# Optimization experiments

Measured on AMD Instinct MI355X. Metric: run time of the kernel, lower is better.

The kernel has to match this reference:

```python
import jax, jax.numpy as jnp
import numpy as np

N_HEADS = 16
ROPE_THETA = 10000.0


def setup_inputs() -> dict:
    key = jax.random.key(0)
    k1, k2, k3 = jax.random.split(key, 3)
    B, T, C = 1, 4096, 1024
    d_k = C // N_HEADS
    x = jax.random.normal(k1, (B, T, C), dtype=jnp.float32)
    # RoPE frequencies: freqs_cis = exp(i * t * theta^{-2j/d_k}), stored as cos/sin
    inv_freq = 1.0 / (ROPE_THETA ** (jnp.arange(0, d_k, 2, dtype=jnp.float32) / d_k))  # (d_k//2,)
    t = jnp.arange(T, dtype=jnp.float32)
    angles = jnp.outer(t, inv_freq)  # (T, d_k//2)
    freqs_cos = jnp.cos(angles)
    freqs_sin = jnp.sin(angles)
    W_attn = jax.random.normal(k2, (C, 3 * C), dtype=jnp.float32) * 0.02  # x @ W_attn == Linear(C,3C,bias=False)
    W_proj = jax.random.normal(k3, (C, C), dtype=jnp.float32) * 0.02
    return {"x": x, "freqs_cos": freqs_cos, "freqs_sin": freqs_sin, "W_attn": W_attn, "W_proj": W_proj}


def _rope(x, cos, sin):
    # x: (B, H, T, d_k); cos/sin: (T, d_k//2). Interleaved-pair rotation
    # matching torch.view_as_complex on (..., d_k//2, 2).
    xr = x.reshape(*x.shape[:-1], -1, 2)
    x0, x1 = xr[..., 0], xr[..., 1]
    c = cos[None, None, :, :]
    s = sin[None, None, :, :]
    o0 = x0 * c - x1 * s
    o1 = x0 * s + x1 * c
    return jnp.stack([o0, o1], axis=-1).reshape(x.shape)


def reference(x, freqs_cos, freqs_sin, W_attn, W_proj):
    B, T, C = x.shape
    H = N_HEADS
    d_k = C // H
    qkv = x @ W_attn  # (B, T, 3C)
    q, k, v = jnp.split(qkv, 3, axis=-1)
    q = q.reshape(B, T, H, d_k).transpose(0, 2, 1, 3)  # (B, H, T, d_k)
    k = k.reshape(B, T, H, d_k).transpose(0, 2, 1, 3)
    v = v.reshape(B, T, H, d_k).transpose(0, 2, 1, 3)
    q = _rope(q, freqs_cos[:T], freqs_sin[:T])
    k = _rope(k, freqs_cos[:T], freqs_sin[:T])
    scale = 1.0 / jnp.sqrt(jnp.asarray(d_k, dtype=x.dtype))
    att = jnp.einsum("bhqd,bhkd->bhqk", q, k) * scale  # (B, H, T, T)
    causal = jnp.tril(jnp.ones((T, T), dtype=bool))
    att = jnp.where(causal[None, None, :, :], att, -jnp.inf)
    att = jax.nn.softmax(att, axis=-1)
    y = jnp.einsum("bhqk,bhkd->bhqd", att, v)  # (B, H, T, d_k)
    y = y.transpose(0, 2, 1, 3).reshape(B, T, C)
    return y @ W_proj
```

## Files before the change

kernel.cpp:

```cpp
#include <hip/hip_runtime.h>

using f32x4  = __attribute__((ext_vector_type(4))) float;
using bf16x4 = __attribute__((ext_vector_type(4))) __bf16;
using bf16x8 = __attribute__((ext_vector_type(8))) __bf16;
using s16x4  = __attribute__((ext_vector_type(4))) short;

__device__ inline void gload16(const void* g, void* l) {
  __builtin_amdgcn_global_load_lds((const __attribute__((address_space(1))) void*)g,
                                   (__attribute__((address_space(3))) void*)l, 16, 0, 0);
}

__device__ inline f32x4 mfma16x16x16bf(bf16x4 a, bf16x4 b, f32x4 c) {
#if __has_builtin(__builtin_amdgcn_mfma_f32_16x16x16_bf16)
  return __builtin_amdgcn_mfma_f32_16x16x16_bf16(a, b, c, 0, 0, 0);
#else
  return __builtin_amdgcn_mfma_f32_16x16x16bf16_1k(__builtin_bit_cast(s16x4, a),
                                                   __builtin_bit_cast(s16x4, b), c, 0, 0, 0);
#endif
}

__global__ __launch_bounds__(256) void pack_bf16_kernel(const float* __restrict__ in,
                                                        __bf16* __restrict__ out, int n4) {
  int i = blockIdx.x * 256 + threadIdx.x;
  if (i >= n4) return;
  f32x4 v = ((const f32x4*)in)[i];
  bf16x4 o;
  o[0] = (__bf16)v[0]; o[1] = (__bf16)v[1]; o[2] = (__bf16)v[2]; o[3] = (__bf16)v[3];
  ((bf16x4*)out)[i] = o;
}

__global__ __launch_bounds__(256) void transpose_bf16_kernel(const float* __restrict__ in,
                                                             __bf16* __restrict__ out,
                                                             int R, int C) {
  __shared__ float tile[32][33];
  int c0 = blockIdx.x * 32, r0 = blockIdx.y * 32;
  int tx = threadIdx.x, ty = threadIdx.y;
  #pragma unroll
  for (int i = 0; i < 32; i += 8)
    tile[ty + i][tx] = in[(size_t)(r0 + ty + i) * C + c0 + tx];
  __syncthreads();
  #pragma unroll
  for (int i = 0; i < 32; i += 8)
    out[(size_t)(c0 + ty + i) * R + r0 + tx] = (__bf16)tile[tx][ty + i];
}

template <typename OUT>
__global__ __launch_bounds__(256) void gemm_bt_kernel(const __bf16* __restrict__ A,
                                                      const __bf16* __restrict__ Bt,
                                                      OUT* __restrict__ C,
                                                      int M, int N, int K) {
  const int nwg = gridDim.x, flat = blockIdx.x;
  const int cpx = nwg >> 3;
  const int wg = (flat & 7) * cpx + (flat >> 3);
  const int nbn = N >> 7;
  const int bn = (wg % nbn) * 128, bm = (wg / nbn) * 128;

  const int tid = threadIdx.x;
  const int lane = tid & 63, wid = tid >> 6;
  const int wm = (wid >> 1) * 64, wn = (wid & 1) * 64;
  const int l15 = lane & 15, lhi = lane >> 4;
  __shared__ __align__(16) __bf16 As[2][4096];
  __shared__ __align__(16) __bf16 Bs[2][4096];
  f32x4 acc[4][4] = {};

  const int rrow = wid * 16 + (lane >> 2);
  const int schunk = lane & 3;

  #define G_STAGE(k0_, b_)                                                              \
    {                                                                                   \
      _Pragma("unroll")                                                                 \
      for (int i_ = 0; i_ < 2; ++i_) {                                                  \
        int row_ = i_ * 64 + rrow;                                                      \
        int lch_ = schunk ^ (row_ & 3);                                                 \
        gload16(A + (size_t)(bm + row_) * K + (k0_) + lch_ * 8,                         \
                (char*)&As[b_][0] + i_ * 4096 + wid * 1024);                            \
        gload16(Bt + (size_t)(bn + row_) * K + (k0_) + lch_ * 8,                        \
                (char*)&Bs[b_][0] + i_ * 4096 + wid * 1024);                            \
      }                                                                                 \
    }

  G_STAGE(0, 0);
  __syncthreads();
  const int nk = K >> 5;
  for (int t = 0; t < nk; ++t) {
    const int cur = t & 1;
    if (t + 1 < nk) G_STAGE((t + 1) * 32, cur ^ 1);
    bf16x8 af[4], bfr[4];
    #pragma unroll
    for (int i = 0; i < 4; ++i) {
      int row = wm + i * 16 + l15;
      af[i] = *(const bf16x8*)&As[cur][row * 32 + ((lhi ^ (row & 3)) * 8)];
    }
    #pragma unroll
    for (int j = 0; j < 4; ++j) {
      int row = wn + j * 16 + l15;
      bfr[j] = *(const bf16x8*)&Bs[cur][row * 32 + ((lhi ^ (row & 3)) * 8)];
    }
    #pragma unroll
    for (int i = 0; i < 4; ++i)
      #pragma unroll
      for (int j = 0; j < 4; ++j)
        acc[i][j] = __builtin_amdgcn_mfma_f32_16x16x32_bf16(af[i], bfr[j], acc[i][j], 0, 0, 0);
    __syncthreads();
  }
  #pragma unroll
  for (int i = 0; i < 4; ++i)
    #pragma unroll
    for (int j = 0; j < 4; ++j)
      #pragma unroll
      for (int r = 0; r < 4; ++r)
        C[(size_t)(bm + wm + i * 16 + lhi * 4 + r) * N + (bn + wn + j * 16 + l15)] =
            (OUT)acc[i][j][r];
  #undef G_STAGE
}

__global__ __launch_bounds__(256) void postproc_kernel(const __bf16* __restrict__ qkv,
                                                       const float* __restrict__ fc,
                                                       const float* __restrict__ fs,
                                                       __bf16* __restrict__ qb,
                                                       __bf16* __restrict__ kst,
                                                       __bf16* __restrict__ vst) {
  const int ktile = blockIdx.x, h = blockIdx.y;
  const int tid = threadIdx.x;
  const int row = tid >> 2, seg = tid & 3;
  const int t = ktile * 64 + row;
  __shared__ __bf16 vt[64][72];

  float cs[8], sn[8];
  #pragma unroll
  for (int p = 0; p < 8; ++p) {
    cs[p] = fc[t * 32 + seg * 8 + p];
    sn[p] = fs[t * 32 + seg * 8 + p];
  }
  const float QS = 0.125f * 1.4426950408889634f;

  {
    const __bf16* src = qkv + (size_t)t * 3072 + h * 64 + seg * 16;
    bf16x8 a = *(const bf16x8*)src, b = *(const bf16x8*)(src + 8);
    float v[16];
    #pragma unroll
    for (int i = 0; i < 8; ++i) { v[i] = (float)a[i]; v[8 + i] = (float)b[i]; }
    __bf16 ob[16];
    #pragma unroll
    for (int p = 0; p < 8; ++p) {
      ob[2 * p]     = (__bf16)((v[2 * p] * cs[p] - v[2 * p + 1] * sn[p]) * QS);
      ob[2 * p + 1] = (__bf16)((v[2 * p] * sn[p] + v[2 * p + 1] * cs[p]) * QS);
    }
    __bf16* dst = qb + (size_t)t * 1024 + h * 64 + seg * 16;
    *(bf16x8*)dst = *(bf16x8*)ob;
    *(bf16x8*)(dst + 8) = *(bf16x8*)(ob + 8);
  }
  {
    const __bf16* src = qkv + (size_t)t * 3072 + 1024 + h * 64 + seg * 16;
    bf16x8 a = *(const bf16x8*)src, b = *(const bf16x8*)(src + 8);
    float v[16];
    #pragma unroll
    for (int i = 0; i < 8; ++i) { v[i] = (float)a[i]; v[8 + i] = (float)b[i]; }
    __bf16 ob[16];
    #pragma unroll
    for (int p = 0; p < 8; ++p) {
      ob[2 * p]     = (__bf16)(v[2 * p] * cs[p] - v[2 * p + 1] * sn[p]);
      ob[2 * p + 1] = (__bf16)(v[2 * p] * sn[p] + v[2 * p + 1] * cs[p]);
    }
    __bf16* kdst = kst + ((size_t)(h * 64 + ktile)) * 4096 + row * 64;
    const int r7 = row & 7;
    *(bf16x8*)(kdst + ((seg * 2) ^ r7) * 8)     = *(bf16x8*)ob;
    *(bf16x8*)(kdst + ((seg * 2 + 1) ^ r7) * 8) = *(bf16x8*)(ob + 8);
  }
  {
    const __bf16* src = qkv + (size_t)t * 3072 + 2048 + h * 64 + seg * 16;
    *(bf16x8*)&vt[row][seg * 16]     = *(const bf16x8*)src;
    *(bf16x8*)&vt[row][seg * 16 + 8] = *(const bf16x8*)(src + 8);
  }
  __syncthreads();
  {
    const int d = tid >> 2, q4 = tid & 3;
    __bf16 tb[16];
    #pragma unroll
    for (int j = 0; j < 16; ++j) tb[j] = vt[q4 * 16 + j][d];
    __bf16* vdst = vst + ((size_t)(h * 64 + ktile)) * 4096 + d * 64;
    const int r7 = d & 7;
    *(bf16x8*)(vdst + ((q4 * 2) ^ r7) * 8)     = *(bf16x8*)tb;
    *(bf16x8*)(vdst + ((q4 * 2 + 1) ^ r7) * 8) = *(bf16x8*)(tb + 8);
  }
}

__global__ __launch_bounds__(256) void fattn_kernel(const __bf16* __restrict__ qb,
                                                    const __bf16* __restrict__ kst,
                                                    const __bf16* __restrict__ vst,
                                                    __bf16* __restrict__ yb) {
  const int b = blockIdx.x;
  const int xcd = b & 7, slot = b >> 3;
  const int head = xcd * 2 + (slot & 1);
  const int qt = 63 - (slot >> 1);
  const int tid = threadIdx.x, lane = tid & 63, w = tid >> 6;
  const int c16 = lane & 15, g = lane >> 4;

  __shared__ __align__(16) __bf16 kls[2][4096];
  __shared__ __align__(16) __bf16 vls[2][4096];

  const __bf16* ktiles = kst + (size_t)head * 64 * 4096;
  const __bf16* vtiles = vst + (size_t)head * 64 * 4096;

  #define F_STAGE(kt_, b_)                                                        \
    {                                                                             \
      const char* kb_ = (const char*)(ktiles + (size_t)(kt_) * 4096);             \
      const char* vb_ = (const char*)(vtiles + (size_t)(kt_) * 4096);             \
      _Pragma("unroll")                                                           \
      for (int i_ = 0; i_ < 2; ++i_) {                                            \
        int off_ = i_ * 4096 + w * 1024;                                          \
        gload16(kb_ + off_ + lane * 16, (char*)&kls[b_][0] + off_);               \
        gload16(vb_ + off_ + lane * 16, (char*)&vls[b_][0] + off_);               \
      }                                                                           \
    }

  const int qw0 = qt * 64 + w * 16;

  bf16x8 qf[2];
  #pragma unroll
  for (int kc = 0; kc < 2; ++kc)
    qf[kc] = *(const bf16x8*)(qb + (size_t)(qw0 + c16) * 1024 + head * 64 + kc * 32 + g * 8);

  f32x4 o[4] = {};
  f32x4 ol = {};
  bf16x4 ones1;
  ones1[0] = ones1[1] = ones1[2] = ones1[3] = (__bf16)1.0f;

  const int m7 = c16 & 7, h2 = g >> 1, lo4 = (g & 1) * 4;
  const __bf16* kp0 = &kls[0][c16 * 64 + ((g ^ m7) * 8)];
  const __bf16* kp1 = &kls[0][c16 * 64 + (((4 + g) ^ m7) * 8)];
  const __bf16* vp0 = &vls[0][c16 * 64 + lo4 + (((0 + h2) ^ m7) * 8)];
  const __bf16* vp1 = &vls[0][c16 * 64 + lo4 + (((2 + h2) ^ m7) * 8)];
  const __bf16* vp2 = &vls[0][c16 * 64 + lo4 + (((4 + h2) ^ m7) * 8)];
  const __bf16* vp3 = &vls[0][c16 * 64 + lo4 + (((6 + h2) ^ m7) * 8)];

  #define F_ONE_ST(B_, st_, vp_)                                                  \
    {                                                                             \
      bf16x4 pv;                                                                  \
      _Pragma("unroll")                                                           \
      for (int r = 0; r < 4; ++r) pv[r] = (__bf16)exp2f(s[st_][r]);               \
      __builtin_amdgcn_s_setprio(1);                                              \
      ol = mfma16x16x16bf(ones1, pv, ol);                                         \
      _Pragma("unroll")                                                           \
      for (int dt = 0; dt < 4; ++dt) {                                            \
        bf16x4 va = *(const bf16x4*)(vp_ + (B_) * 4096 + dt * 1024);              \
        o[dt] = mfma16x16x16bf(va, pv, o[dt]);                                    \
      }                                                                           \
      __builtin_amdgcn_s_setprio(0);                                              \
    }

  #define F_COMPUTE(B_, kt_)                                                      \
    {                                                                             \
      f32x4 s[4];                                                                 \
      __builtin_amdgcn_s_setprio(1);                                              \
      _Pragma("unroll")                                                           \
      for (int st = 0; st < 4; ++st) {                                            \
        bf16x8 ka0 = *(const bf16x8*)(kp0 + (B_) * 4096 + st * 1024);             \
        bf16x8 ka1 = *(const bf16x8*)(kp1 + (B_) * 4096 + st * 1024);             \
        f32x4 z = {};                                                             \
        z = __builtin_amdgcn_mfma_f32_16x16x32_bf16(ka0, qf[0], z, 0, 0, 0);      \
        s[st] = __builtin_amdgcn_mfma_f32_16x16x32_bf16(ka1, qf[1], z, 0, 0, 0);  \
      }                                                                           \
      __builtin_amdgcn_s_setprio(0);                                              \
      if ((kt_) == qt) {                                                          \
        const int qloc = w * 16 + c16;                                            \
        _Pragma("unroll")                                                         \
        for (int st = 0; st < 4; ++st)                                            \
          _Pragma("unroll")                                                       \
          for (int r = 0; r < 4; ++r)                                             \
            if (st * 16 + g * 4 + r > qloc) s[st][r] = -1e30f;                    \
      }                                                                           \
      F_ONE_ST(B_, 0, vp0)                                                        \
      F_ONE_ST(B_, 1, vp1)                                                        \
      F_ONE_ST(B_, 2, vp2)                                                        \
      F_ONE_ST(B_, 3, vp3)                                                        \
    }

  F_STAGE(0, 0);
  __syncthreads();

  int kt = 0;
  while (true) {
    if (kt < qt) F_STAGE(kt + 1, 1);
    F_COMPUTE(0, kt)
    __syncthreads();
    if (kt == qt) break;
    ++kt;
    if (kt < qt) F_STAGE(kt + 1, 0);
    F_COMPUTE(1, kt)
    __syncthreads();
    if (kt == qt) break;
    ++kt;
  }

  const float inv = 1.f / ol[0];
  const int q = qw0 + c16;
  #pragma unroll
  for (int dt = 0; dt < 4; ++dt) {
    bf16x4 ov;
    #pragma unroll
    for (int r = 0; r < 4; ++r) ov[r] = (__bf16)(o[dt][r] * inv);
    *(bf16x4*)(yb + (size_t)q * 1024 + head * 64 + dt * 16 + g * 4) = ov;
  }
  #undef F_STAGE
  #undef F_COMPUTE
  #undef F_ONE_ST
}

extern "C" void kernel_launch(void* const* d_in, const int* in_sizes, int n_in,
                              void* d_out, int out_size, void* d_ws, size_t ws_size,
                              hipStream_t stream) {
  const float* x  = (const float*)d_in[0];
  const float* fc = (const float*)d_in[1];
  const float* fs = (const float*)d_in[2];
  const float* Wa = (const float*)d_in[3];
  const float* Wp = (const float*)d_in[4];
  float* out = (float*)d_out;

  char* ws = (char*)d_ws;
  __bf16* x_bf   = (__bf16*)(ws);
  __bf16* Wa_t   = (__bf16*)(ws + 8388608);
  __bf16* Wp_t   = (__bf16*)(ws + 14680064);
  __bf16* y_bf   = (__bf16*)(ws + 16777216);
  __bf16* qkv_bf = (__bf16*)(ws + 25165824);
  __bf16* kst    = (__bf16*)(ws + 50331648);
  __bf16* vst    = (__bf16*)(ws + 58720256);
  __bf16* q_bf   = x_bf;

  pack_bf16_kernel<<<4096, 256, 0, stream>>>(x, x_bf, 1048576);
  transpose_bf16_kernel<<<dim3(96, 32), dim3(32, 8), 0, stream>>>(Wa, Wa_t, 1024, 3072);
  transpose_bf16_kernel<<<dim3(32, 32), dim3(32, 8), 0, stream>>>(Wp, Wp_t, 1024, 1024);
  gemm_bt_kernel<__bf16><<<768, 256, 0, stream>>>(x_bf, Wa_t, qkv_bf, 4096, 3072, 1024);
  postproc_kernel<<<dim3(64, 16), 256, 0, stream>>>(qkv_bf, fc, fs, q_bf, kst, vst);
  fattn_kernel<<<1024, 256, 0, stream>>>(q_bf, kst, vst, y_bf);
  gemm_bt_kernel<float><<<256, 256, 0, stream>>>(y_bf, Wp_t, out, 4096, 1024, 1024);
}
```

Baseline: 225.1 us.

## Split long causal attention rows across two blocks and fuse prep kernels

Query tiles 31..63 are now each split into two key-range halves handled by separate blocks. Those blocks write unnormalized fp32 partial outputs and row sums, which a new combine kernel adds and normalizes into the bf16 output. This is meant to even out the causal load imbalance, where late query tiles dominate the tail. It also merges the pack and two transpose kernels into one launch to cut launch overhead. In exchange it adds an extra kernel, partial-result traffic, and reuses the qkv buffer region for the partials.

```diff
diff --git a/kernel.cpp b/kernel.cpp
--- a/kernel.cpp
+++ b/kernel.cpp
@@ -19,22 +19,31 @@
 #endif
 }
 
-__global__ __launch_bounds__(256) void pack_bf16_kernel(const float* __restrict__ in,
-                                                        __bf16* __restrict__ out, int n4) {
-  int i = blockIdx.x * 256 + threadIdx.x;
-  if (i >= n4) return;
-  f32x4 v = ((const f32x4*)in)[i];
-  bf16x4 o;
-  o[0] = (__bf16)v[0]; o[1] = (__bf16)v[1]; o[2] = (__bf16)v[2]; o[3] = (__bf16)v[3];
-  ((bf16x4*)out)[i] = o;
-}
-
-__global__ __launch_bounds__(256) void transpose_bf16_kernel(const float* __restrict__ in,
-                                                             __bf16* __restrict__ out,
-                                                             int R, int C) {
+__global__ __launch_bounds__(256) void prep_kernel(const float* __restrict__ x,
+                                                   const float* __restrict__ Wa,
+                                                   const float* __restrict__ Wp,
+                                                   __bf16* __restrict__ x_bf,
+                                                   __bf16* __restrict__ Wa_t,
+                                                   __bf16* __restrict__ Wp_t) {
+  const int b = blockIdx.x, tid = threadIdx.x;
+  if (b < 4096) {
+    int i = b * 256 + tid;
+    f32x4 v = ((const f32x4*)x)[i];
+    bf16x4 o;
+    o[0] = (__bf16)v[0]; o[1] = (__bf16)v[1]; o[2] = (__bf16)v[2]; o[3] = (__bf16)v[3];
+    ((bf16x4*)x_bf)[i] = o;
+    return;
+  }
   __shared__ float tile[32][33];
-  int c0 = blockIdx.x * 32, r0 = blockIdx.y * 32;
-  int tx = threadIdx.x, ty = threadIdx.y;
+  const int tx = tid & 31, ty = tid >> 5;
+  const float* in; __bf16* out; int R, C, c0, r0;
+  if (b < 4096 + 3072) {
+    int bx = b - 4096; in = Wa; out = Wa_t; R = 1024; C = 3072;
+    c0 = (bx % 96) * 32; r0 = (bx / 96) * 32;
+  } else {
+    int bx = b - 7168; in = Wp; out = Wp_t; R = 1024; C = 1024;
+    c0 = (bx & 31) * 32; r0 = (bx >> 5) * 32;
+  }
   #pragma unroll
   for (int i = 0; i < 32; i += 8)
     tile[ty + i][tx] = in[(size_t)(r0 + ty + i) * C + c0 + tx];
@@ -188,11 +197,26 @@
 __global__ __launch_bounds__(256) void fattn_kernel(const __bf16* __restrict__ qb,
                                                     const __bf16* __restrict__ kst,
                                                     const __bf16* __restrict__ vst,
-                                                    __bf16* __restrict__ yb) {
+                                                    __bf16* __restrict__ yb,
+                                                    float* __restrict__ opart,
+                                                    float* __restrict__ lpart) {
   const int b = blockIdx.x;
-  const int xcd = b & 7, slot = b >> 3;
-  const int head = xcd * 2 + (slot & 1);
-  const int qt = 63 - (slot >> 1);
+  const int xcd = b & 7, s = b >> 3;
+  const int head = xcd * 2 + (s & 1);
+  const int slot = s >> 1;
+  int qt, kt0, kt1, part, pid = 0;
+  if (slot < 66) {
+    qt = 63 - (slot >> 1);
+    part = slot & 1;
+    const int h1 = (qt + 1) >> 1;
+    kt0 = part ? h1 : 0;
+    kt1 = part ? qt : h1 - 1;
+    pid = (head * 33 + (qt - 31)) * 2 + part;
+  } else {
+    qt = 30 - (slot - 66);
+    part = -1;
+    kt0 = 0; kt1 = qt;
+  }
   const int tid = threadIdx.x, lane = tid & 63, w = tid >> 6;
   const int c16 = lane & 15, g = lane >> 4;
 
@@ -238,7 +262,7 @@
     {                                                                             \
       bf16x4 pv;                                                                  \
       _Pragma("unroll")                                                           \
-      for (int r = 0; r < 4; ++r) pv[r] = (__bf16)exp2f(s[st_][r]);               \
+      for (int r = 0; r < 4; ++r) pv[r] = (__bf16)exp2f(s_[st_][r]);              \
       __builtin_amdgcn_s_setprio(1);                                              \
       ol = mfma16x16x16bf(ones1, pv, ol);                                         \
       _Pragma("unroll")                                                           \
@@ -251,7 +275,7 @@
 
   #define F_COMPUTE(B_, kt_)                                                      \
     {                                                                             \
-      f32x4 s[4];                                                                 \
+      f32x4 s_[4];                                                                \
       __builtin_amdgcn_s_setprio(1);                                              \
       _Pragma("unroll")                                                           \
       for (int st = 0; st < 4; ++st) {                                            \
@@ -259,7 +283,7 @@
         bf16x8 ka1 = *(const bf16x8*)(kp1 + (B_) * 4096 + st * 1024);             \
         f32x4 z = {};                                                             \
         z = __builtin_amdgcn_mfma_f32_16x16x32_bf16(ka0, qf[0], z, 0, 0, 0);      \
-        s[st] = __builtin_amdgcn_mfma_f32_16x16x32_bf16(ka1, qf[1], z, 0, 0, 0);  \
+        s_[st] = __builtin_amdgcn_mfma_f32_16x16x32_bf16(ka1, qf[1], z, 0, 0, 0); \
       }                                                                           \
       __builtin_amdgcn_s_setprio(0);                                              \
       if ((kt_) == qt) {                                                          \
@@ -268,7 +292,7 @@
         for (int st = 0; st < 4; ++st)                                            \
           _Pragma("unroll")                                                       \
           for (int r = 0; r < 4; ++r)                                             \
-            if (st * 16 + g * 4 + r > qloc) s[st][r] = -1e30f;                    \
+            if (st * 16 + g * 4 + r > qloc) s_[st][r] = -1e30f;                   \
       }                                                                           \
       F_ONE_ST(B_, 0, vp0)                                                        \
       F_ONE_ST(B_, 1, vp1)                                                        \
@@ -276,35 +300,65 @@
       F_ONE_ST(B_, 3, vp3)                                                        \
     }
 
-  F_STAGE(0, 0);
+  F_STAGE(kt0, 0);
   __syncthreads();
 
-  int kt = 0;
+  int kt = kt0;
   while (true) {
-    if (kt < qt) F_STAGE(kt + 1, 1);
+    if (kt < kt1) F_STAGE(kt + 1, 1);
     F_COMPUTE(0, kt)
     __syncthreads();
-    if (kt == qt) break;
+    if (kt == kt1) break;
     ++kt;
-    if (kt < qt) F_STAGE(kt + 1, 0);
+    if (kt < kt1) F_STAGE(kt + 1, 0);
     F_COMPUTE(1, kt)
     __syncthreads();
-    if (kt == qt) break;
+    if (kt == kt1) break;
     ++kt;
   }
 
-  const float inv = 1.f / ol[0];
-  const int q = qw0 + c16;
-  #pragma unroll
-  for (int dt = 0; dt < 4; ++dt) {
-    bf16x4 ov;
-    #pragma unroll
-    for (int r = 0; r < 4; ++r) ov[r] = (__bf16)(o[dt][r] * inv);
-    *(bf16x4*)(yb + (size_t)q * 1024 + head * 64 + dt * 16 + g * 4) = ov;
+  if (part >= 0) {
+    float* Op = opart + (size_t)pid * 4096 + (w * 16 + c16) * 64;
+    #pragma unroll
+    for (int dt = 0; dt < 4; ++dt)
+      *(f32x4*)(Op + dt * 16 + g * 4) = o[dt];
+    if (g == 0) lpart[pid * 64 + w * 16 + c16] = ol[0];
+  } else {
+    const float inv = 1.f / ol[0];
+    const int q = qw0 + c16;
+    #pragma unroll
+    for (int dt = 0; dt < 4; ++dt) {
+      bf16x4 ov;
+      #pragma unroll
+      for (int r = 0; r < 4; ++r) ov[r] = (__bf16)(o[dt][r] * inv);
+      *(bf16x4*)(yb + (size_t)q * 1024 + head * 64 + dt * 16 + g * 4) = ov;
+    }
   }
   #undef F_STAGE
   #undef F_COMPUTE
   #undef F_ONE_ST
+}
+
+__global__ __launch_bounds__(256) void combine_kernel(const float* __restrict__ opart,
+                                                      const float* __restrict__ lpart,
+                                                      __bf16* __restrict__ yb) {
+  const int b = blockIdx.x, tid = threadIdx.x;
+  const int head = b / 33, qt = 31 + (b - head * 33);
+  const int qloc = tid >> 2, d0 = (tid & 3) * 16;
+  const float* O0 = opart + (size_t)(2 * b) * 4096 + qloc * 64 + d0;
+  const float* O1 = O0 + 4096;
+  const float lv = lpart[2 * b * 64 + qloc] + lpart[(2 * b + 1) * 64 + qloc];
+  const float inv = 1.f / lv;
+  __bf16* dst = yb + (size_t)(qt * 64 + qloc) * 1024 + head * 64 + d0;
+  #pragma unroll
+  for (int j = 0; j < 4; ++j) {
+    f32x4 a = *(const f32x4*)(O0 + j * 4);
+    f32x4 c = *(const f32x4*)(O1 + j * 4);
+    bf16x4 ov;
+    #pragma unroll
+    for (int r = 0; r < 4; ++r) ov[r] = (__bf16)((a[r] + c[r]) * inv);
+    *(bf16x4*)(dst + j * 4) = ov;
+  }
 }
 
 extern "C" void kernel_launch(void* const* d_in, const int* in_sizes, int n_in,
@@ -323,15 +377,16 @@
   __bf16* Wp_t   = (__bf16*)(ws + 14680064);
   __bf16* y_bf   = (__bf16*)(ws + 16777216);
   __bf16* qkv_bf = (__bf16*)(ws + 25165824);
+  float*  opart  = (float* )(ws + 25165824);
+  float*  lpart  = (float* )(ws + 42467328);
   __bf16* kst    = (__bf16*)(ws + 50331648);
   __bf16* vst    = (__bf16*)(ws + 58720256);
   __bf16* q_bf   = x_bf;
 
-  pack_bf16_kernel<<<4096, 256, 0, stream>>>(x, x_bf, 1048576);
-  transpose_bf16_kernel<<<dim3(96, 32), dim3(32, 8), 0, stream>>>(Wa, Wa_t, 1024, 3072);
-  transpose_bf16_kernel<<<dim3(32, 32), dim3(32, 8), 0, stream>>>(Wp, Wp_t, 1024, 1024);
+  prep_kernel<<<8192, 256, 0, stream>>>(x, Wa, Wp, x_bf, Wa_t, Wp_t);
   gemm_bt_kernel<__bf16><<<768, 256, 0, stream>>>(x_bf, Wa_t, qkv_bf, 4096, 3072, 1024);
   postproc_kernel<<<dim3(64, 16), 256, 0, stream>>>(qkv_bf, fc, fs, q_bf, kst, vst);
-  fattn_kernel<<<1024, 256, 0, stream>>>(q_bf, kst, vst, y_bf);
+  fattn_kernel<<<1552, 256, 0, stream>>>(q_bf, kst, vst, y_bf, opart, lpart);
+  combine_kernel<<<528, 256, 0, stream>>>(opart, lpart, y_bf);
   gemm_bt_kernel<float><<<256, 256, 0, stream>>>(y_bf, Wp_t, out, 4096, 1024, 1024);
 }
```

Result: slower. 239.6 us (+6.4%).

## Merge prep kernels into one launch and use partial vmcnt waits in pipelines

Applied to the files above, without the earlier changes.

Combines the x bf16 pack and the two weight transposes into a single prep kernel, removing two launches. In the GEMM and flash-attention loops, __syncthreads is replaced with explicit s_waitcnt vmcnt(4) plus s_barrier, so the prefetch of the next stage can stay in flight while the current LDS buffer is consumed. This depends on vmcnt counts matching the number of loads issued per stage; a wrong count would create a race.

```diff
diff --git a/kernel.cpp b/kernel.cpp
--- a/kernel.cpp
+++ b/kernel.cpp
@@ -19,22 +19,35 @@
 #endif
 }
 
-__global__ __launch_bounds__(256) void pack_bf16_kernel(const float* __restrict__ in,
-                                                        __bf16* __restrict__ out, int n4) {
-  int i = blockIdx.x * 256 + threadIdx.x;
-  if (i >= n4) return;
-  f32x4 v = ((const f32x4*)in)[i];
-  bf16x4 o;
-  o[0] = (__bf16)v[0]; o[1] = (__bf16)v[1]; o[2] = (__bf16)v[2]; o[3] = (__bf16)v[3];
-  ((bf16x4*)out)[i] = o;
-}
-
-__global__ __launch_bounds__(256) void transpose_bf16_kernel(const float* __restrict__ in,
-                                                             __bf16* __restrict__ out,
-                                                             int R, int C) {
+#define VM_WAIT4 asm volatile("s_waitcnt vmcnt(4)" ::: "memory")
+#define VM_WAIT0 asm volatile("s_waitcnt vmcnt(0)" ::: "memory")
+#define BARRIER  __builtin_amdgcn_s_barrier()
+
+__global__ __launch_bounds__(256) void prep_kernel(const float* __restrict__ x,
+                                                   const float* __restrict__ Wa,
+                                                   const float* __restrict__ Wp,
+                                                   __bf16* __restrict__ x_bf,
+                                                   __bf16* __restrict__ Wa_t,
+                                                   __bf16* __restrict__ Wp_t) {
+  const int b = blockIdx.x, tid = threadIdx.x;
+  if (b < 4096) {
+    int i = b * 256 + tid;
+    f32x4 v = ((const f32x4*)x)[i];
+    bf16x4 o;
+    o[0] = (__bf16)v[0]; o[1] = (__bf16)v[1]; o[2] = (__bf16)v[2]; o[3] = (__bf16)v[3];
+    ((bf16x4*)x_bf)[i] = o;
+    return;
+  }
   __shared__ float tile[32][33];
-  int c0 = blockIdx.x * 32, r0 = blockIdx.y * 32;
-  int tx = threadIdx.x, ty = threadIdx.y;
+  const int tx = tid & 31, ty = tid >> 5;
+  const float* in; __bf16* out; int R, C, c0, r0;
+  if (b < 4096 + 3072) {
+    int bx = b - 4096; in = Wa; out = Wa_t; R = 1024; C = 3072;
+    c0 = (bx % 96) * 32; r0 = (bx / 96) * 32;
+  } else {
+    int bx = b - 7168; in = Wp; out = Wp_t; R = 1024; C = 1024;
+    c0 = (bx & 31) * 32; r0 = (bx >> 5) * 32;
+  }
   #pragma unroll
   for (int i = 0; i < 32; i += 8)
     tile[ty + i][tx] = in[(size_t)(r0 + ty + i) * C + c0 + tx];
@@ -80,11 +93,11 @@
     }
 
   G_STAGE(0, 0);
-  __syncthreads();
   const int nk = K >> 5;
   for (int t = 0; t < nk; ++t) {
     const int cur = t & 1;
-    if (t + 1 < nk) G_STAGE((t + 1) * 32, cur ^ 1);
+    if (t + 1 < nk) { G_STAGE((t + 1) * 32, cur ^ 1); VM_WAIT4; } else { VM_WAIT0; }
+    BARRIER;
     bf16x8 af[4], bfr[4];
     #pragma unroll
     for (int i = 0; i < 4; ++i) {
@@ -101,7 +114,7 @@
       #pragma unroll
       for (int j = 0; j < 4; ++j)
         acc[i][j] = __builtin_amdgcn_mfma_f32_16x16x32_bf16(af[i], bfr[j], acc[i][j], 0, 0, 0);
-    __syncthreads();
+    BARRIER;
   }
   #pragma unroll
   for (int i = 0; i < 4; ++i)
@@ -238,7 +251,7 @@
     {                                                                             \
       bf16x4 pv;                                                                  \
       _Pragma("unroll")                                                           \
-      for (int r = 0; r < 4; ++r) pv[r] = (__bf16)exp2f(s[st_][r]);               \
+      for (int r = 0; r < 4; ++r) pv[r] = (__bf16)exp2f(s_[st_][r]);              \
       __builtin_amdgcn_s_setprio(1);                                              \
       ol = mfma16x16x16bf(ones1, pv, ol);                                         \
       _Pragma("unroll")                                                           \
@@ -251,7 +264,7 @@
 
   #define F_COMPUTE(B_, kt_)                                                      \
     {                                                                             \
-      f32x4 s[4];                                                                 \
+      f32x4 s_[4];                                                                \
       __builtin_amdgcn_s_setprio(1);                                              \
       _Pragma("unroll")                                                           \
       for (int st = 0; st < 4; ++st) {                                            \
@@ -259,7 +272,7 @@
         bf16x8 ka1 = *(const bf16x8*)(kp1 + (B_) * 4096 + st * 1024);             \
         f32x4 z = {};                                                             \
         z = __builtin_amdgcn_mfma_f32_16x16x32_bf16(ka0, qf[0], z, 0, 0, 0);      \
-        s[st] = __builtin_amdgcn_mfma_f32_16x16x32_bf16(ka1, qf[1], z, 0, 0, 0);  \
+        s_[st] = __builtin_amdgcn_mfma_f32_16x16x32_bf16(ka1, qf[1], z, 0, 0, 0); \
       }                                                                           \
       __builtin_amdgcn_s_setprio(0);                                              \
       if ((kt_) == qt) {                                                          \
@@ -268,7 +281,7 @@
         for (int st = 0; st < 4; ++st)                                            \
           _Pragma("unroll")                                                       \
           for (int r = 0; r < 4; ++r)                                             \
-            if (st * 16 + g * 4 + r > qloc) s[st][r] = -1e30f;                    \
+            if (st * 16 + g * 4 + r > qloc) s_[st][r] = -1e30f;                   \
       }                                                                           \
       F_ONE_ST(B_, 0, vp0)                                                        \
       F_ONE_ST(B_, 1, vp1)                                                        \
@@ -277,18 +290,19 @@
     }
 
   F_STAGE(0, 0);
-  __syncthreads();
 
   int kt = 0;
   while (true) {
-    if (kt < qt) F_STAGE(kt + 1, 1);
+    if (kt < qt) { F_STAGE(kt + 1, 1); VM_WAIT4; } else { VM_WAIT0; }
+    BARRIER;
     F_COMPUTE(0, kt)
-    __syncthreads();
+    BARRIER;
     if (kt == qt) break;
     ++kt;
-    if (kt < qt) F_STAGE(kt + 1, 0);
+    if (kt < qt) { F_STAGE(kt + 1, 0); VM_WAIT4; } else { VM_WAIT0; }
+    BARRIER;
     F_COMPUTE(1, kt)
-    __syncthreads();
+    BARRIER;
     if (kt == qt) break;
     ++kt;
   }
@@ -327,9 +341,7 @@
   __bf16* vst    = (__bf16*)(ws + 58720256);
   __bf16* q_bf   = x_bf;
 
-  pack_bf16_kernel<<<4096, 256, 0, stream>>>(x, x_bf, 1048576);
-  transpose_bf16_kernel<<<dim3(96, 32), dim3(32, 8), 0, stream>>>(Wa, Wa_t, 1024, 3072);
-  transpose_bf16_kernel<<<dim3(32, 32), dim3(32, 8), 0, stream>>>(Wp, Wp_t, 1024, 1024);
+  prep_kernel<<<8192, 256, 0, stream>>>(x, Wa, Wp, x_bf, Wa_t, Wp_t);
   gemm_bt_kernel<__bf16><<<768, 256, 0, stream>>>(x_bf, Wa_t, qkv_bf, 4096, 3072, 1024);
   postproc_kernel<<<dim3(64, 16), 256, 0, stream>>>(qkv_bf, fc, fs, q_bf, kst, vst);
   fattn_kernel<<<1024, 256, 0, stream>>>(q_bf, kst, vst, y_bf);
```

Result: slower. 229.7 us (+2.0%).
